# Kernel tuning notes

Measured on AMD Instinct MI355X. Metric: run time of the kernel, lower is better.

## Reference

```python
import jax, jax.numpy as jnp
import numpy as np

D = 3
BS = 64
T = 2048


def _fnn(x, w1, b1, w2, b2):
    # FNNnew: fc2(tanh(fc1(x))) * exp(-5*x); x: (T,1) -> (T,)
    z = jnp.tanh(x @ w1.T + b1) @ w2.T + b2
    return (z * jnp.exp(-5.0 * x))[:, 0]


def setup_inputs() -> dict:
    key = jax.random.key(0)
    ks = jax.random.split(key, 32)
    inp = {"x_data": jax.random.normal(ks[0], (BS, T, 2), dtype=jnp.float32)}
    inp["A1"] = jax.random.normal(ks[1], (D, D), dtype=jnp.float32)
    inp["A2"] = jax.random.normal(ks[2], (D, D), dtype=jnp.float32)
    i = 3
    for n in ("f", "g", "fp", "gp"):
        inp[n + "_w1"] = jax.random.normal(ks[i], (5, 1), dtype=jnp.float32) * 0.5; i += 1
        inp[n + "_b1"] = jax.random.normal(ks[i], (5,), dtype=jnp.float32) * 0.1; i += 1
        inp[n + "_w2"] = jax.random.normal(ks[i], (1, 5), dtype=jnp.float32) * 0.5; i += 1
        inp[n + "_b2"] = jax.random.normal(ks[i], (1,), dtype=jnp.float32) * 0.1; i += 1
    return inp


def reference(x_data, A1, A2, f_w1, f_b1, f_w2, f_b2, g_w1, g_b1, g_w2, g_b2,
              fp_w1, fp_b1, fp_w2, fp_b2, gp_w1, gp_b1, gp_w2, gp_b2):
    bs, t_len, _ = x_data.shape
    d = A1.shape[0]
    t = jnp.arange(t_len, dtype=jnp.float32)[:, None]
    f_arr = _fnn(t, f_w1, f_b1, f_w2, f_b2)[::-1]
    fp_arr = _fnn(t, fp_w1, fp_b1, fp_w2, fp_b2)[::-1]
    g_arr = _fnn(t, g_w1, g_b1, g_w2, g_b2)
    gp_arr = _fnn(t, gp_w1, gp_b1, gp_w2, gp_b2)
    # time-domain zero-pad then FFT (length 3T-2)
    Hf = jnp.fft.fft(jnp.pad(f_arr, (t_len - 1, t_len - 1)))
    Hfp = jnp.fft.fft(jnp.pad(fp_arr, (t_len - 1, t_len - 1)))
    Hg = jnp.fft.fft(jnp.pad(g_arr, (t_len - 1, t_len - 1)))
    Hgp = jnp.fft.fft(jnp.pad(gp_arr, (t_len - 1, t_len - 1)))
    # PathDev: X_t = X_{t-1} @ expm(A1s*z1_t + A2s*z2_t), X_0 = I
    A1s = A1 - A1.T
    A2s = A2 - A2.T
    G = A1s * x_data[..., 0, None, None] + A2s * x_data[..., 1, None, None]  # (bs,T,d,d)
    M = jax.vmap(jax.scipy.linalg.expm)(G.reshape(-1, d, d)).reshape(bs, t_len, d, d)

    X0 = jnp.broadcast_to(jnp.eye(d, dtype=x_data.dtype), (bs, d, d))

    def step(X, Mt):
        Xn = jnp.einsum('bij,bjk->bik', X, Mt)
        return Xn, Xn

    _, Xs = jax.lax.scan(step, X0, jnp.moveaxis(M[:, 1:], 0, 1))
    A = jnp.concatenate([X0[:, None], jnp.moveaxis(Xs, 0, 1)], axis=1)  # (bs,T,d,d)
    B = jnp.linalg.inv(A)
    Xr = A.reshape(bs, t_len, d * d)
    Xir = B.reshape(bs, t_len, d * d)
    # original pads the FFT output (frequency-domain padding) before multiply
    pad_t = lambda z: jnp.pad(z, ((0, 0), (t_len - 1, t_len - 1), (0, 0)))
    AA_fft = pad_t(jnp.fft.fft(Xir, axis=1))  # (bs, 3T-2, d^2)
    AB_fft = pad_t(jnp.fft.fft(Xr, axis=1))
    brd = lambda h: h[None, :, None]
    AA = jnp.fft.ifft(AA_fft * brd(Hf), axis=1)
    AB = jnp.fft.ifft(AB_fft * brd(Hg), axis=1)
    BA = jnp.fft.ifft(AA_fft * brd(Hfp), axis=1)
    BB = jnp.fft.ifft(AB_fft * brd(Hgp), axis=1)
    out = (AA * AB + BA * BB)[:, 2 * t_len - 2:, :]  # (bs,T,d^2)
    return out.reshape(bs, t_len, d, d).real
```

## Files before the change

### kernel.cpp

```cpp
#include <hip/hip_runtime.h>
#include <math.h>

#define TN 2048
#define NF 4096
#define NB 64
#define LF 6142LL
#define L2F 12284LL
#define PI_D 3.14159265358979323846264338327950288
#define C8 0.70710678118654752440084436210485
#define K16A 0.92387953251128675612818318939678828682
#define K16B 0.38268343236508977172845998403039886676
#define C8f   0.70710678118654752440f
#define K16Af 0.92387953251128675613f
#define K16Bf 0.38268343236508977173f

typedef double2 cpx;
typedef float2 cf;

__device__ __forceinline__ cpx cmk(double a, double b){ cpx r; r.x=a; r.y=b; return r; }
__device__ __forceinline__ cpx cadd(cpx a, cpx b){ return cmk(a.x+b.x, a.y+b.y); }
__device__ __forceinline__ cpx csub(cpx a, cpx b){ return cmk(a.x-b.x, a.y-b.y); }
__device__ __forceinline__ cpx cmul(cpx a, cpx b){ return cmk(a.x*b.x - a.y*b.y, a.x*b.y + a.y*b.x); }
__device__ __forceinline__ cpx cmulc(cpx a, cpx b){ return cmk(a.x*b.x + a.y*b.y, a.y*b.x - a.x*b.y); }
__device__ __forceinline__ cf c2s(cpx a){ cf r; r.x=(float)a.x; r.y=(float)a.y; return r; }

__device__ __forceinline__ cf cfmk(float a, float b){ cf r; r.x=a; r.y=b; return r; }
__device__ __forceinline__ cf cfadd(cf a, cf b){ return cfmk(a.x+b.x, a.y+b.y); }
__device__ __forceinline__ cf cfsub(cf a, cf b){ return cfmk(a.x-b.x, a.y-b.y); }
__device__ __forceinline__ cf cfmul(cf a, cf b){ return cfmk(a.x*b.x - a.y*b.y, a.x*b.y + a.y*b.x); }
__device__ __forceinline__ cf cfmulc(cf a, cf b){ return cfmk(a.x*b.x + a.y*b.y, a.y*b.x - a.x*b.y); }

__device__ __forceinline__ int SW(int i){ return i ^ ((i >> 3) & 7) ^ ((i >> 6) & 7); }
__device__ __forceinline__ int SWP(int i){ return i ^ ((i >> 4) & 15) ^ ((i >> 8) & 15); }

__device__ __forceinline__ void wsync(){
  __builtin_amdgcn_wave_barrier();
  asm volatile("s_waitcnt lgkmcnt(0)" ::: "memory");
  __builtin_amdgcn_wave_barrier();
}

__device__ __forceinline__ void fft8_bc(cpx* a){
  cpx u, v, d;
  u=a[0]; v=a[2]; a[0]=cadd(u,v); a[2]=csub(u,v);
  u=a[1]; v=a[3]; a[1]=cadd(u,v); d=csub(u,v); a[3]=cmk(d.y, -d.x);
  u=a[4]; v=a[6]; a[4]=cadd(u,v); a[6]=csub(u,v);
  u=a[5]; v=a[7]; a[5]=cadd(u,v); d=csub(u,v); a[7]=cmk(d.y, -d.x);
  u=a[0]; v=a[1]; a[0]=cadd(u,v); a[1]=csub(u,v);
  u=a[2]; v=a[3]; a[2]=cadd(u,v); a[3]=csub(u,v);
  u=a[4]; v=a[5]; a[4]=cadd(u,v); a[5]=csub(u,v);
  u=a[6]; v=a[7]; a[6]=cadd(u,v); a[7]=csub(u,v);
}
__device__ __forceinline__ void fft8(cpx* a){
  cpx u, v, d;
  u=a[0]; v=a[4]; a[0]=cadd(u,v); a[4]=csub(u,v);
  u=a[1]; v=a[5]; a[1]=cadd(u,v); d=csub(u,v); a[5]=cmk(C8*(d.x+d.y), C8*(d.y-d.x));
  u=a[2]; v=a[6]; a[2]=cadd(u,v); d=csub(u,v); a[6]=cmk(d.y, -d.x);
  u=a[3]; v=a[7]; a[3]=cadd(u,v); d=csub(u,v); a[7]=cmk(C8*(d.y-d.x), -C8*(d.x+d.y));
  fft8_bc(a);
}
__device__ __forceinline__ void fft16(cpx* a){
  cpx u, v, d;
  u=a[0]; v=a[8];  a[0]=cadd(u,v); a[8] = csub(u,v);
  u=a[1]; v=a[9];  a[1]=cadd(u,v); d=csub(u,v); a[9]  = cmk(K16A*d.x + K16B*d.y, K16A*d.y - K16B*d.x);
  u=a[2]; v=a[10]; a[2]=cadd(u,v); d=csub(u,v); a[10] = cmk(C8*(d.x+d.y), C8*(d.y-d.x));
  u=a[3]; v=a[11]; a[3]=cadd(u,v); d=csub(u,v); a[11] = cmk(K16B*d.x + K16A*d.y, K16B*d.y - K16A*d.x);
  u=a[4]; v=a[12]; a[4]=cadd(u,v); d=csub(u,v); a[12] = cmk(d.y, -d.x);
  u=a[5]; v=a[13]; a[5]=cadd(u,v); d=csub(u,v); a[13] = cmk(K16A*d.y - K16B*d.x, -(K16A*d.x + K16B*d.y));
  u=a[6]; v=a[14]; a[6]=cadd(u,v); d=csub(u,v); a[14] = cmk(C8*(d.y-d.x), -C8*(d.x+d.y));
  u=a[7]; v=a[15]; a[7]=cadd(u,v); d=csub(u,v); a[15] = cmk(K16B*d.y - K16A*d.x, -(K16A*d.y + K16B*d.x));
  fft8(a); fft8(a+8);
}

__device__ __forceinline__ void fft8s_bc(cf* a){
  cf u, v, d;
  u=a[0]; v=a[2]; a[0]=cfadd(u,v); a[2]=cfsub(u,v);
  u=a[1]; v=a[3]; a[1]=cfadd(u,v); d=cfsub(u,v); a[3]=cfmk(d.y, -d.x);
  u=a[4]; v=a[6]; a[4]=cfadd(u,v); a[6]=cfsub(u,v);
  u=a[5]; v=a[7]; a[5]=cfadd(u,v); d=cfsub(u,v); a[7]=cfmk(d.y, -d.x);
  u=a[0]; v=a[1]; a[0]=cfadd(u,v); a[1]=cfsub(u,v);
  u=a[2]; v=a[3]; a[2]=cfadd(u,v); a[3]=cfsub(u,v);
  u=a[4]; v=a[5]; a[4]=cfadd(u,v); a[5]=cfsub(u,v);
  u=a[6]; v=a[7]; a[6]=cfadd(u,v); a[7]=cfsub(u,v);
}
__device__ __forceinline__ void fft8s(cf* a){
  cf u, v, d;
  u=a[0]; v=a[4]; a[0]=cfadd(u,v); a[4]=cfsub(u,v);
  u=a[1]; v=a[5]; a[1]=cfadd(u,v); d=cfsub(u,v); a[5]=cfmk(C8f*(d.x+d.y), C8f*(d.y-d.x));
  u=a[2]; v=a[6]; a[2]=cfadd(u,v); d=cfsub(u,v); a[6]=cfmk(d.y, -d.x);
  u=a[3]; v=a[7]; a[3]=cfadd(u,v); d=cfsub(u,v); a[7]=cfmk(C8f*(d.y-d.x), -C8f*(d.x+d.y));
  fft8s_bc(a);
}
__device__ __forceinline__ void ifft8s(cf* a){
  cf u, v, t;
  u=a[0]; v=a[1]; a[0]=cfadd(u,v); a[1]=cfsub(u,v);
  u=a[2]; v=a[3]; a[2]=cfadd(u,v); a[3]=cfsub(u,v);
  u=a[4]; v=a[5]; a[4]=cfadd(u,v); a[5]=cfsub(u,v);
  u=a[6]; v=a[7]; a[6]=cfadd(u,v); a[7]=cfsub(u,v);
  u=a[0]; v=a[2]; a[0]=cfadd(u,v); a[2]=cfsub(u,v);
  u=a[1]; t=a[3]; v=cfmk(-t.y, t.x); a[1]=cfadd(u,v); a[3]=cfsub(u,v);
  u=a[4]; v=a[6]; a[4]=cfadd(u,v); a[6]=cfsub(u,v);
  u=a[5]; t=a[7]; v=cfmk(-t.y, t.x); a[5]=cfadd(u,v); a[7]=cfsub(u,v);
  u=a[0]; v=a[4]; a[0]=cfadd(u,v); a[4]=cfsub(u,v);
  u=a[1]; t=a[5]; v=cfmk(C8f*(t.x-t.y), C8f*(t.x+t.y)); a[1]=cfadd(u,v); a[5]=cfsub(u,v);
  u=a[2]; t=a[6]; v=cfmk(-t.y, t.x); a[2]=cfadd(u,v); a[6]=cfsub(u,v);
  u=a[3]; t=a[7]; v=cfmk(-C8f*(t.x+t.y), C8f*(t.x-t.y)); a[3]=cfadd(u,v); a[7]=cfsub(u,v);
}
__device__ __forceinline__ void fft4s(cf* a){
  cf u, v, d;
  u=a[0]; v=a[2]; a[0]=cfadd(u,v); a[2]=cfsub(u,v);
  u=a[1]; v=a[3]; a[1]=cfadd(u,v); d=cfsub(u,v); a[3]=cfmk(d.y, -d.x);
  u=a[0]; v=a[1]; a[0]=cfadd(u,v); a[1]=cfsub(u,v);
  u=a[2]; v=a[3]; a[2]=cfadd(u,v); a[3]=cfsub(u,v);
}
__device__ __forceinline__ void ffts16(cf* a){
  cf u, v, d;
  u=a[0]; v=a[8];  a[0]=cfadd(u,v); a[8] = cfsub(u,v);
  u=a[1]; v=a[9];  a[1]=cfadd(u,v); d=cfsub(u,v); a[9]  = cfmk(K16Af*d.x + K16Bf*d.y, K16Af*d.y - K16Bf*d.x);
  u=a[2]; v=a[10]; a[2]=cfadd(u,v); d=cfsub(u,v); a[10] = cfmk(C8f*(d.x+d.y), C8f*(d.y-d.x));
  u=a[3]; v=a[11]; a[3]=cfadd(u,v); d=cfsub(u,v); a[11] = cfmk(K16Bf*d.x + K16Af*d.y, K16Bf*d.y - K16Af*d.x);
  u=a[4]; v=a[12]; a[4]=cfadd(u,v); d=cfsub(u,v); a[12] = cfmk(d.y, -d.x);
  u=a[5]; v=a[13]; a[5]=cfadd(u,v); d=cfsub(u,v); a[13] = cfmk(K16Af*d.y - K16Bf*d.x, -(K16Af*d.x + K16Bf*d.y));
  u=a[6]; v=a[14]; a[6]=cfadd(u,v); d=cfsub(u,v); a[14] = cfmk(C8f*(d.y-d.x), -C8f*(d.x+d.y));
  u=a[7]; v=a[15]; a[7]=cfadd(u,v); d=cfsub(u,v); a[15] = cfmk(K16Bf*d.y - K16Af*d.x, -(K16Af*d.y + K16Bf*d.x));
  fft8s(a); fft8s(a+8);
}
__device__ __forceinline__ void ffts16h(cf* a){
  a[8]  = a[0];
  a[9]  = cfmk(K16Af*a[1].x + K16Bf*a[1].y, K16Af*a[1].y - K16Bf*a[1].x);
  a[10] = cfmk(C8f*(a[2].x+a[2].y), C8f*(a[2].y-a[2].x));
  a[11] = cfmk(K16Bf*a[3].x + K16Af*a[3].y, K16Bf*a[3].y - K16Af*a[3].x);
  a[12] = cfmk(a[4].y, -a[4].x);
  a[13] = cfmk(K16Af*a[5].y - K16Bf*a[5].x, -(K16Af*a[5].x + K16Bf*a[5].y));
  a[14] = cfmk(C8f*(a[6].y-a[6].x), -C8f*(a[6].x+a[6].y));
  a[15] = cfmk(K16Bf*a[7].y - K16Af*a[7].x, -(K16Af*a[7].y + K16Bf*a[7].x));
  fft8s(a); fft8s(a+8);
}
__device__ __forceinline__ void iffts16(cf* a){
  ifft8s(a); ifft8s(a+8);
  cf t, E;
  E=a[0]; t=a[8];                                                                   a[0]=cfadd(E,t); a[8] =cfsub(E,t);
  E=a[1]; t=cfmk(K16Af*a[9].x - K16Bf*a[9].y,  K16Af*a[9].y + K16Bf*a[9].x);        a[1]=cfadd(E,t); a[9] =cfsub(E,t);
  E=a[2]; t=cfmk(C8f*(a[10].x - a[10].y),      C8f*(a[10].x + a[10].y));            a[2]=cfadd(E,t); a[10]=cfsub(E,t);
  E=a[3]; t=cfmk(K16Bf*a[11].x - K16Af*a[11].y, K16Bf*a[11].y + K16Af*a[11].x);     a[3]=cfadd(E,t); a[11]=cfsub(E,t);
  E=a[4]; t=cfmk(-a[12].y, a[12].x);                                                a[4]=cfadd(E,t); a[12]=cfsub(E,t);
  E=a[5]; t=cfmk(-(K16Bf*a[13].x) - K16Af*a[13].y, K16Af*a[13].x - K16Bf*a[13].y);  a[5]=cfadd(E,t); a[13]=cfsub(E,t);
  E=a[6]; t=cfmk(-C8f*(a[14].x + a[14].y),     C8f*(a[14].x - a[14].y));            a[6]=cfadd(E,t); a[14]=cfsub(E,t);
  E=a[7]; t=cfmk(-(K16Af*a[15].x) - K16Bf*a[15].y, K16Bf*a[15].x - K16Af*a[15].y);  a[7]=cfadd(E,t); a[15]=cfsub(E,t);
}
__device__ __forceinline__ void iffts16h(cf* a){
  ifft8s(a); ifft8s(a+8);
  cf t;
  t=a[8];                                                                  a[0]=cfadd(a[0],t);
  t=cfmk(K16Af*a[9].x - K16Bf*a[9].y,  K16Af*a[9].y + K16Bf*a[9].x);       a[1]=cfadd(a[1],t);
  t=cfmk(C8f*(a[10].x - a[10].y),      C8f*(a[10].x + a[10].y));           a[2]=cfadd(a[2],t);
  t=cfmk(K16Bf*a[11].x - K16Af*a[11].y, K16Bf*a[11].y + K16Af*a[11].x);    a[3]=cfadd(a[3],t);
  t=cfmk(-a[12].y, a[12].x);                                               a[4]=cfadd(a[4],t);
  t=cfmk(-(K16Bf*a[13].x) - K16Af*a[13].y, K16Af*a[13].x - K16Bf*a[13].y); a[5]=cfadd(a[5],t);
  t=cfmk(-C8f*(a[14].x + a[14].y),     C8f*(a[14].x - a[14].y));           a[6]=cfadd(a[6],t);
  t=cfmk(-(K16Af*a[15].x) - K16Bf*a[15].y, K16Bf*a[15].x - K16Af*a[15].y); a[7]=cfadd(a[7],t);
}

__global__ __launch_bounds__(256) void k_prep(
    const float* fw1, const float* fb1, const float* fw2, const float* fb2,
    const float* gw1, const float* gb1, const float* gw2, const float* gb2,
    const float* pw1, const float* pb1, const float* pw2, const float* pb2,
    const float* qw1, const float* qb1, const float* qw2, const float* qb2,
    double* arr, cpx* tw, cf* tw32, cpx* Q, cpx* g2)
{
  int gid = blockIdx.x * 256 + threadIdx.x;
  if (gid < 4096){
    double s, c;
    sincos(-2.0 * PI_D * (double)gid / 4096.0, &s, &c);
    tw[gid] = cmk(c, s);
    tw32[gid] = cfmk((float)c, (float)s);
  }
  if (gid < 2048){
    long long i = gid;
    double s, c;
    long long a = ((2LL * TN - 2) * i) % LF;
    long long b = (i * i) % L2F;
    long long comb = (2 * a + b) % L2F;
    sincos(PI_D * (double)comb / (double)LF, &s, &c);
    Q[gid] = cmk(c, s);
    long long a2 = ((2LL * TN - 2 + i) * (TN - 1)) % LF;
    long long comb2 = (2 * a2 + b) % L2F;
    double phi = PI_D * (double)comb2 / (double)LF;
    double scale = 1.0 / ((double)LF * (double)LF) / (4096.0 * 4096.0);
    sincos(2.0 * phi, &s, &c);
    g2[gid] = cmk(c * scale, s * scale);
  }
  int fid = gid >> 11;
  int m = gid & (TN - 1);
  const float *W1, *B1, *W2, *B2;
  if (fid == 0){ W1=fw1; B1=fb1; W2=fw2; B2=fb2; }
  else if (fid == 1){ W1=gw1; B1=gb1; W2=gw2; B2=gb2; }
  else if (fid == 2){ W1=pw1; B1=pb1; W2=pw2; B2=pb2; }
  else { W1=qw1; B1=qb1; W2=qw2; B2=qb2; }
  int s = (fid == 0 || fid == 2) ? (TN - 1 - m) : m;
  double sv = (double)s;
  double z = (double)B2[0];
  #pragma unroll
  for (int h = 0; h < 5; h++)
    z += (double)W2[h] * tanh(sv * (double)W1[h] + (double)B1[h]);
  arr[fid * TN + m] = z * exp(-5.0 * sv);
}

__device__ __forceinline__ void mat_mul3(double* D, const double* A, const double* B){
  double r[9];
  #pragma unroll
  for (int i = 0; i < 3; i++)
    #pragma unroll
    for (int j = 0; j < 3; j++)
      r[i*3+j] = A[i*3]*B[j] + A[i*3+1]*B[3+j] + A[i*3+2]*B[6+j];
  #pragma unroll
  for (int k = 0; k < 9; k++) D[k] = r[k];
}
__device__ __forceinline__ void rod3(double* M, const double* a1, const double* a2,
                                     double z1, double z2){
  double G[9];
  #pragma unroll
  for (int k = 0; k < 9; k++) G[k] = a1[k]*z1 + a2[k]*z2;
  double wx = G[7], wy = G[2], wz = G[3];
  double th2 = wx*wx + wy*wy + wz*wz;
  double sa, cb;
  if (th2 < 1e-12){ sa = 1.0 - th2/6.0; cb = 0.5 - th2/24.0; }
  else { double th = sqrt(th2); sa = sin(th)/th; cb = (1.0 - cos(th))/th2; }
  double w[3] = {wx, wy, wz};
  #pragma unroll
  for (int i = 0; i < 3; i++)
    #pragma unroll
    for (int j = 0; j < 3; j++){
      double v = sa * G[i*3+j] + cb * (w[i]*w[j]);
      if (i == j) v += 1.0 - cb * th2;
      M[i*3+j] = v;
    }
}

__global__ __launch_bounds__(256) void k_front(
    const float* x, const float* A1f, const float* A2f,
    const double* arr, const cpx* Q, const cpx* tw,
    cf* HsQ, float* Asc, cf* chatp)
{
  __shared__ double smem[8192];
  int tid = threadIdx.x;
  int bid = blockIdx.x;
  if (bid < 256){
    cpx* part = (cpx*)smem;
    int f = bid >> 6;
    int jbase = (bid & 63) * 32;
    int chunk = tid & 7;
    int jl = tid >> 3;
    long long j = jbase + jl;
    long long jj = j + TN - 1;
    double s, c;
    sincos(-2.0 * PI_D * (double)jj / (double)LF, &s, &c);
    cpx W = cmk(c, s);
    long long m0 = (long long)chunk * 256;
    long long p0 = ((m0 + TN - 1) * jj) % LF;
    sincos(-2.0 * PI_D * (double)p0 / (double)LF, &s, &c);
    cpx ph = cmk(c, s);
    const double* a = arr + f * TN;
    cpx acc = cmk(0.0, 0.0);
    for (int m = (int)m0; m < (int)m0 + 256; m++){
      double av = a[m];
      acc.x += av * ph.x;
      acc.y += av * ph.y;
      ph = cmul(ph, W);
    }
    part[tid] = acc;
    __syncthreads();
    if (chunk == 0){
      cpx tot = cmk(0.0, 0.0);
      for (int q = 0; q < 8; q++) tot = cadd(tot, part[(jl << 3) + q]);
      HsQ[f * TN + (int)j] = c2s(cmul(tot, Q[j]));
    }
  } else if (bid < 320){
    int b = bid - 256;
    double (*S)[9] = (double(*)[9])smem;
    int k = tid;
    double a1[9], a2[9];
    #pragma unroll
    for (int i = 0; i < 3; i++)
      #pragma unroll
      for (int j = 0; j < 3; j++){
        a1[i*3+j] = (double)A1f[i*3+j] - (double)A1f[j*3+i];
        a2[i*3+j] = (double)A2f[i*3+j] - (double)A2f[j*3+i];
      }
    const float* xb = x + (size_t)b * TN * 2;
    double C[9] = {1,0,0, 0,1,0, 0,0,1};
    for (int i = 0; i < 8; i++){
      int t = k * 8 + i;
      if (t >= 1){
        double M[9];
        rod3(M, a1, a2, (double)xb[2*t], (double)xb[2*t+1]);
        mat_mul3(C, C, M);
      }
    }
    #pragma unroll
    for (int q = 0; q < 9; q++) S[k][q] = C[q];
    __syncthreads();
    for (int ofs = 1; ofs < 256; ofs <<= 1){
      double Lm[9], Rm[9];
      bool act = (k >= ofs);
      if (act){
        #pragma unroll
        for (int q = 0; q < 9; q++){ Lm[q] = S[k-ofs][q]; Rm[q] = S[k][q]; }
      }
      __syncthreads();
      if (act){
        double P[9];
        mat_mul3(P, Lm, Rm);
        #pragma unroll
        for (int q = 0; q < 9; q++) S[k][q] = P[q];
      }
      __syncthreads();
    }
    double P[9];
    if (k == 0){
      P[0]=1; P[1]=0; P[2]=0; P[3]=0; P[4]=1; P[5]=0; P[6]=0; P[7]=0; P[8]=1;
    } else {
      #pragma unroll
      for (int q = 0; q < 9; q++) P[q] = S[k-1][q];
    }
    for (int i = 0; i < 8; i++){
      int t = k * 8 + i;
      if (t >= 1){
        double M[9];
        rod3(M, a1, a2, (double)xb[2*t], (double)xb[2*t+1]);
        mat_mul3(P, P, M);
      }
      #pragma unroll
      for (int q = 0; q < 9; q++)
        Asc[(((size_t)b * 9 + q) << 11) + t] = (float)P[q];
    }
  } else {
    cpx* buf = (cpx*)smem;
    const int R16[16] = {0,8,4,12,2,10,6,14,1,9,5,13,3,11,7,15};
    for (int mq = tid; mq < NF; mq += 256){
      long long mm = (mq <= 2048) ? mq : (NF - mq);
      long long qq = (mm * mm) % L2F;
      double s, c;
      sincos(-PI_D * (double)qq / (double)LF, &s, &c);
      buf[SW(mq)] = cmk(c, s);
    }
    __syncthreads();
    {
      cpx a[16];
      #pragma unroll
      for (int k = 0; k < 16; k++) a[k] = buf[SW(tid + (k << 8))];
      fft16(a);
      #pragma unroll
      for (int q = 0; q < 16; q++){
        int d = R16[q]; cpx v = a[q];
        if (d) v = cmul(v, tw[tid * d]);
        buf[SW(tid + (d << 8))] = v;
      }
    }
    __syncthreads();
    {
      int m2 = tid & 15, base2 = ((tid >> 4) << 8) + m2;
      cpx a[16];
      #pragma unroll
      for (int k = 0; k < 16; k++) a[k] = buf[SW(base2 + (k << 4))];
      fft16(a);
      #pragma unroll
      for (int q = 0; q < 16; q++){
        int d = R16[q]; cpx v = a[q];
        if (d) v = cmul(v, tw[(m2 * d) << 4]);
        buf[SW(base2 + (d << 4))] = v;
      }
    }
    __syncthreads();
    {
      cpx a[16];
      #pragma unroll
      for (int k = 0; k < 16; k++) a[k] = buf[SW((tid << 4) + k)];
      fft16(a);
      #pragma unroll
      for (int q = 0; q < 16; q++)
        chatp[(R16[q] << 8) | tid] = c2s(a[q]);
    }
  }
}

__global__ __launch_bounds__(256, 4) void k_fft_u(const float* Asc, const cf* tw32, cf* U){
  __shared__ cf buf[TN];
  int pos = threadIdx.x;
  int b = blockIdx.x / 5, p = blockIdx.x % 5;
  int c0 = 2 * p;
  bool dual = (p < 4);
  const float* s0 = Asc + (((size_t)b * 9 + c0) << 11);
  const float* s1 = Asc + (((size_t)b * 9 + (dual ? c0 + 1 : c0)) << 11);
  const int R8[8] = {0,4,2,6,1,5,3,7};
  {
    cf a[8];
    #pragma unroll
    for (int j = 0; j < 8; j++){
      int idx = pos + (j << 8);
      a[j] = cfmk(s0[idx], dual ? s1[idx] : 0.0f);
    }
    fft8s(a);
    #pragma unroll
    for (int q = 0; q < 8; q++){
      int k = R8[q]; cf v = a[q];
      if (k) v = cfmul(v, tw32[(pos * k) << 1]);
      buf[SW(pos + (k << 8))] = v;
    }
  }
  __syncthreads();
  int l = pos & 63;
  int ll = l & 31;
  int segb = ((((pos >> 6) << 1) + (l >> 5)) << 8);
  {
    int base = segb + ll;
    cf a[8];
    #pragma unroll
    for (int j = 0; j < 8; j++) a[j] = buf[SW(base + (j << 5))];
    fft8s(a);
    #pragma unroll
    for (int q = 0; q < 8; q++){
      int k = R8[q]; cf v = a[q];
      if (k) v = cfmul(v, tw32[(ll * k) << 4]);
      buf[SW(base + (k << 5))] = v;
    }
  }
  wsync();
  {
    int base = segb + ((ll >> 2) << 5) + (ll & 3);
    cf a[8];
    #pragma unroll
    for (int j = 0; j < 8; j++) a[j] = buf[SW(base + (j << 2))];
    fft8s(a);
    #pragma unroll
    for (int q = 0; q < 8; q++){
      int k = R8[q]; cf v = a[q];
      if (k) v = cfmul(v, tw32[((ll & 3) * k) << 7]);
      buf[SW(base + (k << 2))] = v;
    }
  }
  wsync();
  {
    const int R4[4] = {0,2,1,3};
    #pragma unroll
    for (int h = 0; h < 2; h++){
      int base = segb + (((ll << 1) + h) << 2);
      cf a4[4];
      #pragma unroll
      for (int j = 0; j < 4; j++) a4[j] = buf[SW(base + j)];
      fft4s(a4);
      #pragma unroll
      for (int q = 0; q < 4; q++) buf[SW(base + R4[q])] = a4[q];
    }
  }
  __syncthreads();
  cf* dst0 = U + (((size_t)b * 9 + c0) << 11);
  cf* dst1 = U + (((size_t)b * 9 + c0 + 1) << 11);
  #pragma unroll
  for (int ii = 0; ii < 8; ii++){
    int f = pos + (ii << 8);
    int s  = ((f & 7) << 8) + (((f >> 3) & 7) << 5) + (((f >> 6) & 7) << 2) + (f >> 9);
    int m  = (TN - f) & (TN - 1);
    int sm = ((m & 7) << 8) + (((m >> 3) & 7) << 5) + (((m >> 6) & 7) << 2) + (m >> 9);
    cf Z = buf[SW(s)], Zm = buf[SW(sm)];
    dst0[f] = cfmk(0.5f * (Z.x + Zm.x), 0.5f * (Z.y - Zm.y));
    if (dual)
      dst1[f] = cfmk(0.5f * (Z.y + Zm.y), 0.5f * (Zm.x - Z.x));
  }
}

__global__ __launch_bounds__(256, 2) void k_czt(const cf* U, const cf* HsQ, const cf* tw32,
                                                const cf* chatp, const cpx* g2, float* Rst){
  __shared__ float4 bufp[NF];
  int gb = blockIdx.x;
  int pair = gb & 1;
  int bc = gb >> 1;
  int b = bc / 9, c = bc % 9;
  int ct = (c % 3) * 3 + (c / 3);
  const cf* Us0 = U + ((size_t)b * 9 + ct) * TN;
  const cf* Us1 = U + ((size_t)b * 9 + c)  * TN;
  const cf* H0 = HsQ + ((size_t)(pair << 1) << 11);
  const cf* H1 = HsQ + ((size_t)((pair << 1) | 1) << 11);
  int t = threadIdx.x;
  int m = t & 15;
  int base2 = ((t >> 4) << 8) + m;
  int base3 = t << 4;
  const int R16[16] = {0,8,4,12,2,10,6,14,1,9,5,13,3,11,7,15};

  cf a[16], bb[16];
  #pragma unroll
  for (int k = 0; k < 8; k++){
    a[k]  = cfmul(Us0[t + (k << 8)], H0[t + (k << 8)]);
    bb[k] = cfmul(Us1[t + (k << 8)], H1[t + (k << 8)]);
  }
  ffts16h(a); ffts16h(bb);
  #pragma unroll
  for (int q = 0; q < 16; q++){
    int d = R16[q];
    cf va = a[q], vb = bb[q];
    if (d){ cf tv = tw32[t * d]; va = cfmul(va, tv); vb = cfmul(vb, tv); }
    bufp[SWP(t + (d << 8))] = make_float4(va.x, va.y, vb.x, vb.y);
  }
  __syncthreads();
  #pragma unroll
  for (int k = 0; k < 16; k++){
    float4 p = bufp[SWP(base2 + (k << 4))];
    a[k]  = cfmk(p.x, p.y);
    bb[k] = cfmk(p.z, p.w);
  }
  ffts16(a); ffts16(bb);
  #pragma unroll
  for (int q = 0; q < 16; q++){
    int d = R16[q];
    cf va = a[q], vb = bb[q];
    if (d){ cf tv = tw32[(m * d) << 4]; va = cfmul(va, tv); vb = cfmul(vb, tv); }
    bufp[SWP(base2 + (d << 4))] = make_float4(va.x, va.y, vb.x, vb.y);
  }
  wsync();
  #pragma unroll
  for (int k = 0; k < 16; k++){
    float4 p = bufp[SWP(base3 + k)];
    a[k]  = cfmk(p.x, p.y);
    bb[k] = cfmk(p.z, p.w);
  }
  ffts16(a); ffts16(bb);
  #pragma unroll
  for (int q = 0; q < 16; q++){
    cf ch = chatp[(R16[q] << 8) | t];
    a[q] = cfmul(a[q], ch);
    bb[q] = cfmul(bb[q], ch);
  }
  iffts16(a); iffts16(bb);
  #pragma unroll
  for (int k = 0; k < 16; k++)
    bufp[SWP(base3 + k)] = make_float4(a[k].x, a[k].y, bb[k].x, bb[k].y);
  wsync();
  #pragma unroll
  for (int q = 0; q < 16; q++){
    int d = R16[q];
    float4 p = bufp[SWP(base2 + (d << 4))];
    cf va = cfmk(p.x, p.y), vb = cfmk(p.z, p.w);
    if (d){ cf tv = tw32[(m * d) << 4]; va = cfmulc(va, tv); vb = cfmulc(vb, tv); }
    a[q] = va; bb[q] = vb;
  }
  iffts16(a); iffts16(bb);
  #pragma unroll
  for (int k = 0; k < 16; k++)
    bufp[SWP(base2 + (k << 4))] = make_float4(a[k].x, a[k].y, bb[k].x, bb[k].y);
  __syncthreads();
  #pragma unroll
  for (int q = 0; q < 16; q++){
    int d = R16[q];
    float4 p = bufp[SWP(t + (d << 8))];
    cf va = cfmk(p.x, p.y), vb = cfmk(p.z, p.w);
    if (d){ cf tv = tw32[t * d]; va = cfmulc(va, tv); vb = cfmulc(vb, tv); }
    a[q] = va; bb[q] = vb;
  }
  iffts16h(a); iffts16h(bb);
  size_t rb = ((size_t)(pair * (NB * 9) + bc) << 11);
  #pragma unroll
  for (int j = 0; j < 8; j++){
    int r = t + (j << 8);
    double ax = (double)a[j].x, ay = (double)a[j].y;
    double bx = (double)bb[j].x, by = (double)bb[j].y;
    double prx = ax * bx - ay * by;
    double pry = ax * by + ay * bx;
    cpx g = g2[r];
    Rst[rb + r] = (float)(prx * g.x - pry * g.y);
  }
}

__global__ __launch_bounds__(256) void k_out(const float* Rst, float* out){
  __shared__ float ld[9][513];
  int b = blockIdx.x >> 2;
  int r0 = (blockIdx.x & 3) << 9;
  for (int idx = threadIdx.x; idx < 9 * 512; idx += 256){
    int cc = idx >> 9, r = idx & 511;
    size_t o0 = ((size_t)(b * 9 + cc) << 11) + r0 + r;
    ld[cc][r] = Rst[o0] + Rst[o0 + ((size_t)(NB * 9) << 11)];
  }
  __syncthreads();
  for (int idx = threadIdx.x; idx < 512 * 9; idx += 256){
    int r = idx / 9, cc = idx - 9 * r;
    out[((size_t)b * TN + r0 + r) * 9 + cc] = ld[cc][r];
  }
}

extern "C" void kernel_launch(void* const* d_in, const int* in_sizes, int n_in,
                              void* d_out, int out_size, void* d_ws, size_t ws_size,
                              hipStream_t stream){
  const float* x  = (const float*)d_in[0];
  const float* A1 = (const float*)d_in[1];
  const float* A2 = (const float*)d_in[2];
  const float* fpar[16];
  for (int i = 0; i < 16; i++) fpar[i] = (const float*)d_in[3 + i];
  float* out = (float*)d_out;

  double* ws = (double*)d_ws;
  size_t o = 0;
  double* arr  = ws + o;         o += 4 * TN;
  cf* HsQ      = (cf*)(ws + o);  o += 4 * TN;
  cpx* tw      = (cpx*)(ws + o); o += 2 * NF;
  cf* tw32     = (cf*)(ws + o);  o += NF;
  cf* chatp    = (cf*)(ws + o);  o += NF;
  cpx* Q       = (cpx*)(ws + o); o += 2 * TN;
  cpx* g2      = (cpx*)(ws + o); o += 2 * TN;
  double* uni  = ws + o;         o += (size_t)NB * TN * 9;
  float* Asc   = (float*)uni;
  float* Rst   = (float*)uni;
  cf* U        = (cf*)(ws + o);  o += (size_t)NB * 9 * TN;

  k_prep<<<32, 256, 0, stream>>>(fpar[0], fpar[1], fpar[2], fpar[3],
                                 fpar[4], fpar[5], fpar[6], fpar[7],
                                 fpar[8], fpar[9], fpar[10], fpar[11],
                                 fpar[12], fpar[13], fpar[14], fpar[15],
                                 arr, tw, tw32, Q, g2);
  k_front<<<321, 256, 0, stream>>>(x, A1, A2, arr, Q, tw, HsQ, Asc, chatp);
  k_fft_u<<<NB * 5, 256, 0, stream>>>(Asc, tw32, U);
  k_czt<<<NB * 9 * 2, 256, 0, stream>>>(U, HsQ, tw32, chatp, g2, Rst);
  k_out<<<NB * 4, 256, 0, stream>>>(Rst, out);
}
```

Baseline: 188.8 us.

## Fuse output transpose into CZT kernel via atomics; reorder front blocks; float filter array

Removes the separate k_out kernel and its intermediate Rst buffer. The two CZT halves now atomically add their results directly into the zeroed output, in the strided final layout, which adds a memset and uncoalesced atomics in exchange. The front kernel puts the long serial path-development blocks first so they are scheduled before the filter DFT blocks. The NN filter evaluation now runs in float rather than double, which slightly reduces precision.

```diff
diff --git a/kernel.cpp b/kernel.cpp
--- a/kernel.cpp
+++ b/kernel.cpp
@@ -165,7 +165,7 @@
     const float* gw1, const float* gb1, const float* gw2, const float* gb2,
     const float* pw1, const float* pb1, const float* pw2, const float* pb2,
     const float* qw1, const float* qb1, const float* qw2, const float* qb2,
-    double* arr, cpx* tw, cf* tw32, cpx* Q, cpx* g2)
+    float* arr, cpx* tw, cf* tw32, cpx* Q, cpx* g2)
 {
   int gid = blockIdx.x * 256 + threadIdx.x;
   if (gid < 4096){
@@ -197,12 +197,12 @@
   else if (fid == 2){ W1=pw1; B1=pb1; W2=pw2; B2=pb2; }
   else { W1=qw1; B1=qb1; W2=qw2; B2=qb2; }
   int s = (fid == 0 || fid == 2) ? (TN - 1 - m) : m;
-  double sv = (double)s;
-  double z = (double)B2[0];
+  float sv = (float)s;
+  float z = B2[0];
   #pragma unroll
   for (int h = 0; h < 5; h++)
-    z += (double)W2[h] * tanh(sv * (double)W1[h] + (double)B1[h]);
-  arr[fid * TN + m] = z * exp(-5.0 * sv);
+    z += W2[h] * tanhf(sv * W1[h] + B1[h]);
+  arr[fid * TN + m] = z * expf(-5.0f * sv);
 }
 
 __device__ __forceinline__ void mat_mul3(double* D, const double* A, const double* B){
@@ -238,44 +238,14 @@
 
 __global__ __launch_bounds__(256) void k_front(
     const float* x, const float* A1f, const float* A2f,
-    const double* arr, const cpx* Q, const cpx* tw,
+    const float* arr, const cpx* Q, const cpx* tw,
     cf* HsQ, float* Asc, cf* chatp)
 {
   __shared__ double smem[8192];
   int tid = threadIdx.x;
   int bid = blockIdx.x;
-  if (bid < 256){
-    cpx* part = (cpx*)smem;
-    int f = bid >> 6;
-    int jbase = (bid & 63) * 32;
-    int chunk = tid & 7;
-    int jl = tid >> 3;
-    long long j = jbase + jl;
-    long long jj = j + TN - 1;
-    double s, c;
-    sincos(-2.0 * PI_D * (double)jj / (double)LF, &s, &c);
-    cpx W = cmk(c, s);
-    long long m0 = (long long)chunk * 256;
-    long long p0 = ((m0 + TN - 1) * jj) % LF;
-    sincos(-2.0 * PI_D * (double)p0 / (double)LF, &s, &c);
-    cpx ph = cmk(c, s);
-    const double* a = arr + f * TN;
-    cpx acc = cmk(0.0, 0.0);
-    for (int m = (int)m0; m < (int)m0 + 256; m++){
-      double av = a[m];
-      acc.x += av * ph.x;
-      acc.y += av * ph.y;
-      ph = cmul(ph, W);
-    }
-    part[tid] = acc;
-    __syncthreads();
-    if (chunk == 0){
-      cpx tot = cmk(0.0, 0.0);
-      for (int q = 0; q < 8; q++) tot = cadd(tot, part[(jl << 3) + q]);
-      HsQ[f * TN + (int)j] = c2s(cmul(tot, Q[j]));
-    }
-  } else if (bid < 320){
-    int b = bid - 256;
+  if (bid < 64){
+    int b = bid;
     double (*S)[9] = (double(*)[9])smem;
     int k = tid;
     double a1[9], a2[9];
@@ -333,7 +303,7 @@
       for (int q = 0; q < 9; q++)
         Asc[(((size_t)b * 9 + q) << 11) + t] = (float)P[q];
     }
-  } else {
+  } else if (bid == 64){
     cpx* buf = (cpx*)smem;
     const int R16[16] = {0,8,4,12,2,10,6,14,1,9,5,13,3,11,7,15};
     for (int mq = tid; mq < NF; mq += 256){
@@ -379,6 +349,37 @@
       #pragma unroll
       for (int q = 0; q < 16; q++)
         chatp[(R16[q] << 8) | tid] = c2s(a[q]);
+    }
+  } else {
+    int hb = bid - 65;
+    cpx* part = (cpx*)smem;
+    int f = hb >> 6;
+    int jbase = (hb & 63) * 32;
+    int chunk = tid & 7;
+    int jl = tid >> 3;
+    long long j = jbase + jl;
+    long long jj = j + TN - 1;
+    double s, c;
+    sincos(-2.0 * PI_D * (double)jj / (double)LF, &s, &c);
+    cpx W = cmk(c, s);
+    long long m0 = (long long)chunk * 256;
+    long long p0 = ((m0 + TN - 1) * jj) % LF;
+    sincos(-2.0 * PI_D * (double)p0 / (double)LF, &s, &c);
+    cpx ph = cmk(c, s);
+    const float* a = arr + f * TN;
+    cpx acc = cmk(0.0, 0.0);
+    for (int m = (int)m0; m < (int)m0 + 256; m++){
+      double av = (double)a[m];
+      acc.x += av * ph.x;
+      acc.y += av * ph.y;
+      ph = cmul(ph, W);
+    }
+    part[tid] = acc;
+    __syncthreads();
+    if (chunk == 0){
+      cpx tot = cmk(0.0, 0.0);
+      for (int q = 0; q < 8; q++) tot = cadd(tot, part[(jl << 3) + q]);
+      HsQ[f * TN + (int)j] = c2s(cmul(tot, Q[j]));
     }
   }
 }
@@ -469,7 +470,7 @@
 }
 
 __global__ __launch_bounds__(256, 2) void k_czt(const cf* U, const cf* HsQ, const cf* tw32,
-                                                const cf* chatp, const cpx* g2, float* Rst){
+                                                const cf* chatp, const cpx* g2, float* out){
   __shared__ float4 bufp[NF];
   int gb = blockIdx.x;
   int pair = gb & 1;
@@ -556,7 +557,7 @@
     a[q] = va; bb[q] = vb;
   }
   iffts16h(a); iffts16h(bb);
-  size_t rb = ((size_t)(pair * (NB * 9) + bc) << 11);
+  float* ob = out + (size_t)b * TN * 9 + c;
   #pragma unroll
   for (int j = 0; j < 8; j++){
     int r = t + (j << 8);
@@ -565,23 +566,7 @@
     double prx = ax * bx - ay * by;
     double pry = ax * by + ay * bx;
     cpx g = g2[r];
-    Rst[rb + r] = (float)(prx * g.x - pry * g.y);
-  }
-}
-
-__global__ __launch_bounds__(256) void k_out(const float* Rst, float* out){
-  __shared__ float ld[9][513];
-  int b = blockIdx.x >> 2;
-  int r0 = (blockIdx.x & 3) << 9;
-  for (int idx = threadIdx.x; idx < 9 * 512; idx += 256){
-    int cc = idx >> 9, r = idx & 511;
-    size_t o0 = ((size_t)(b * 9 + cc) << 11) + r0 + r;
-    ld[cc][r] = Rst[o0] + Rst[o0 + ((size_t)(NB * 9) << 11)];
-  }
-  __syncthreads();
-  for (int idx = threadIdx.x; idx < 512 * 9; idx += 256){
-    int r = idx / 9, cc = idx - 9 * r;
-    out[((size_t)b * TN + r0 + r) * 9 + cc] = ld[cc][r];
+    atomicAdd(ob + (size_t)r * 9, (float)(prx * g.x - pry * g.y));
   }
 }
 
@@ -597,17 +582,17 @@
 
   double* ws = (double*)d_ws;
   size_t o = 0;
-  double* arr  = ws + o;         o += 4 * TN;
+  float* arr   = (float*)(ws + o); o += 2 * TN;
   cf* HsQ      = (cf*)(ws + o);  o += 4 * TN;
   cpx* tw      = (cpx*)(ws + o); o += 2 * NF;
   cf* tw32     = (cf*)(ws + o);  o += NF;
   cf* chatp    = (cf*)(ws + o);  o += NF;
   cpx* Q       = (cpx*)(ws + o); o += 2 * TN;
   cpx* g2      = (cpx*)(ws + o); o += 2 * TN;
-  double* uni  = ws + o;         o += (size_t)NB * TN * 9;
-  float* Asc   = (float*)uni;
-  float* Rst   = (float*)uni;
+  float* Asc   = (float*)(ws + o); o += (size_t)NB * TN * 9 / 2;
   cf* U        = (cf*)(ws + o);  o += (size_t)NB * 9 * TN;
+
+  hipMemsetAsync(d_out, 0, out_size, stream);
 
   k_prep<<<32, 256, 0, stream>>>(fpar[0], fpar[1], fpar[2], fpar[3],
                                  fpar[4], fpar[5], fpar[6], fpar[7],
@@ -616,6 +601,5 @@
                                  arr, tw, tw32, Q, g2);
   k_front<<<321, 256, 0, stream>>>(x, A1, A2, arr, Q, tw, HsQ, Asc, chatp);
   k_fft_u<<<NB * 5, 256, 0, stream>>>(Asc, tw32, U);
-  k_czt<<<NB * 9 * 2, 256, 0, stream>>>(U, HsQ, tw32, chatp, g2, Rst);
-  k_out<<<NB * 4, 256, 0, stream>>>(Rst, out);
-}
+  k_czt<<<NB * 9 * 2, 256, 0, stream>>>(U, HsQ, tw32, chatp, g2, out);
+}
```

Result: slower. 216.0 us (+14.4%).

## Fold prep kernel into front kernel, computing FNN arrays and twiddles per block

Applied to the files above, without the earlier changes.

Removes the separate k_prep launch. Its work is spread across k_front blocks: each H-block recomputes its FNN array in float into shared memory, computes the Q phase inline, and uses on-the-fly double twiddles. Dedicated blocks generate tw32 and g2. This drops one kernel launch and its serial dependency, and removes the global arr, tw and Q buffers. In exchange the FNN work is repeated in every block, and the FNN now runs in float instead of double, which may change accuracy.

```diff
diff --git a/kernel.cpp b/kernel.cpp
--- a/kernel.cpp
+++ b/kernel.cpp
@@ -29,6 +29,12 @@
 __device__ __forceinline__ cf cfsub(cf a, cf b){ return cfmk(a.x-b.x, a.y-b.y); }
 __device__ __forceinline__ cf cfmul(cf a, cf b){ return cfmk(a.x*b.x - a.y*b.y, a.x*b.y + a.y*b.x); }
 __device__ __forceinline__ cf cfmulc(cf a, cf b){ return cfmk(a.x*b.x + a.y*b.y, a.y*b.x - a.x*b.y); }
+
+__device__ __forceinline__ cpx twd64(int idx){
+  double s, c;
+  sincos(-2.0 * PI_D * (double)idx / 4096.0, &s, &c);
+  return cmk(c, s);
+}
 
 __device__ __forceinline__ int SW(int i){ return i ^ ((i >> 3) & 7) ^ ((i >> 6) & 7); }
 __device__ __forceinline__ int SWP(int i){ return i ^ ((i >> 4) & 15) ^ ((i >> 8) & 15); }
@@ -160,51 +166,6 @@
   t=cfmk(-(K16Af*a[15].x) - K16Bf*a[15].y, K16Bf*a[15].x - K16Af*a[15].y); a[7]=cfadd(a[7],t);
 }
 
-__global__ __launch_bounds__(256) void k_prep(
-    const float* fw1, const float* fb1, const float* fw2, const float* fb2,
-    const float* gw1, const float* gb1, const float* gw2, const float* gb2,
-    const float* pw1, const float* pb1, const float* pw2, const float* pb2,
-    const float* qw1, const float* qb1, const float* qw2, const float* qb2,
-    double* arr, cpx* tw, cf* tw32, cpx* Q, cpx* g2)
-{
-  int gid = blockIdx.x * 256 + threadIdx.x;
-  if (gid < 4096){
-    double s, c;
-    sincos(-2.0 * PI_D * (double)gid / 4096.0, &s, &c);
-    tw[gid] = cmk(c, s);
-    tw32[gid] = cfmk((float)c, (float)s);
-  }
-  if (gid < 2048){
-    long long i = gid;
-    double s, c;
-    long long a = ((2LL * TN - 2) * i) % LF;
-    long long b = (i * i) % L2F;
-    long long comb = (2 * a + b) % L2F;
-    sincos(PI_D * (double)comb / (double)LF, &s, &c);
-    Q[gid] = cmk(c, s);
-    long long a2 = ((2LL * TN - 2 + i) * (TN - 1)) % LF;
-    long long comb2 = (2 * a2 + b) % L2F;
-    double phi = PI_D * (double)comb2 / (double)LF;
-    double scale = 1.0 / ((double)LF * (double)LF) / (4096.0 * 4096.0);
-    sincos(2.0 * phi, &s, &c);
-    g2[gid] = cmk(c * scale, s * scale);
-  }
-  int fid = gid >> 11;
-  int m = gid & (TN - 1);
-  const float *W1, *B1, *W2, *B2;
-  if (fid == 0){ W1=fw1; B1=fb1; W2=fw2; B2=fb2; }
-  else if (fid == 1){ W1=gw1; B1=gb1; W2=gw2; B2=gb2; }
-  else if (fid == 2){ W1=pw1; B1=pb1; W2=pw2; B2=pb2; }
-  else { W1=qw1; B1=qb1; W2=qw2; B2=qb2; }
-  int s = (fid == 0 || fid == 2) ? (TN - 1 - m) : m;
-  double sv = (double)s;
-  double z = (double)B2[0];
-  #pragma unroll
-  for (int h = 0; h < 5; h++)
-    z += (double)W2[h] * tanh(sv * (double)W1[h] + (double)B1[h]);
-  arr[fid * TN + m] = z * exp(-5.0 * sv);
-}
-
 __device__ __forceinline__ void mat_mul3(double* D, const double* A, const double* B){
   double r[9];
   #pragma unroll
@@ -238,44 +199,17 @@
 
 __global__ __launch_bounds__(256) void k_front(
     const float* x, const float* A1f, const float* A2f,
-    const double* arr, const cpx* Q, const cpx* tw,
-    cf* HsQ, float* Asc, cf* chatp)
+    const float* fw1, const float* fb1, const float* fw2, const float* fb2,
+    const float* gw1, const float* gb1, const float* gw2, const float* gb2,
+    const float* pw1, const float* pb1, const float* pw2, const float* pb2,
+    const float* qw1, const float* qb1, const float* qw2, const float* qb2,
+    cf* HsQ, float* Asc, cf* chatp, cf* tw32, cpx* g2)
 {
   __shared__ double smem[8192];
   int tid = threadIdx.x;
   int bid = blockIdx.x;
-  if (bid < 256){
-    cpx* part = (cpx*)smem;
-    int f = bid >> 6;
-    int jbase = (bid & 63) * 32;
-    int chunk = tid & 7;
-    int jl = tid >> 3;
-    long long j = jbase + jl;
-    long long jj = j + TN - 1;
-    double s, c;
-    sincos(-2.0 * PI_D * (double)jj / (double)LF, &s, &c);
-    cpx W = cmk(c, s);
-    long long m0 = (long long)chunk * 256;
-    long long p0 = ((m0 + TN - 1) * jj) % LF;
-    sincos(-2.0 * PI_D * (double)p0 / (double)LF, &s, &c);
-    cpx ph = cmk(c, s);
-    const double* a = arr + f * TN;
-    cpx acc = cmk(0.0, 0.0);
-    for (int m = (int)m0; m < (int)m0 + 256; m++){
-      double av = a[m];
-      acc.x += av * ph.x;
-      acc.y += av * ph.y;
-      ph = cmul(ph, W);
-    }
-    part[tid] = acc;
-    __syncthreads();
-    if (chunk == 0){
-      cpx tot = cmk(0.0, 0.0);
-      for (int q = 0; q < 8; q++) tot = cadd(tot, part[(jl << 3) + q]);
-      HsQ[f * TN + (int)j] = c2s(cmul(tot, Q[j]));
-    }
-  } else if (bid < 320){
-    int b = bid - 256;
+  if (bid < 64){
+    int b = bid;
     double (*S)[9] = (double(*)[9])smem;
     int k = tid;
     double a1[9], a2[9];
@@ -333,7 +267,7 @@
       for (int q = 0; q < 9; q++)
         Asc[(((size_t)b * 9 + q) << 11) + t] = (float)P[q];
     }
-  } else {
+  } else if (bid == 64){
     cpx* buf = (cpx*)smem;
     const int R16[16] = {0,8,4,12,2,10,6,14,1,9,5,13,3,11,7,15};
     for (int mq = tid; mq < NF; mq += 256){
@@ -352,7 +286,7 @@
       #pragma unroll
       for (int q = 0; q < 16; q++){
         int d = R16[q]; cpx v = a[q];
-        if (d) v = cmul(v, tw[tid * d]);
+        if (d) v = cmul(v, twd64(tid * d));
         buf[SW(tid + (d << 8))] = v;
       }
     }
@@ -366,7 +300,7 @@
       #pragma unroll
       for (int q = 0; q < 16; q++){
         int d = R16[q]; cpx v = a[q];
-        if (d) v = cmul(v, tw[(m2 * d) << 4]);
+        if (d) v = cmul(v, twd64((m2 * d) << 4));
         buf[SW(base2 + (d << 4))] = v;
       }
     }
@@ -379,6 +313,75 @@
       #pragma unroll
       for (int q = 0; q < 16; q++)
         chatp[(R16[q] << 8) | tid] = c2s(a[q]);
+    }
+  } else if (bid == 65){
+    for (int i = tid; i < NF; i += 256){
+      double s, c;
+      sincos(-2.0 * PI_D * (double)i / 4096.0, &s, &c);
+      tw32[i] = cfmk((float)c, (float)s);
+    }
+    for (int gi = tid; gi < TN; gi += 256){
+      long long i = gi;
+      double s, c;
+      long long b2 = (i * i) % L2F;
+      long long a2 = ((2LL * TN - 2 + i) * (TN - 1)) % LF;
+      long long comb2 = (2 * a2 + b2) % L2F;
+      double phi = PI_D * (double)comb2 / (double)LF;
+      double scale = 1.0 / ((double)LF * (double)LF) / (4096.0 * 4096.0);
+      sincos(2.0 * phi, &s, &c);
+      g2[gi] = cmk(c * scale, s * scale);
+    }
+  } else {
+    int hb = bid - 66;
+    int f = hb >> 6;
+    float* arrF = (float*)smem;
+    cpx* part = (cpx*)(smem + 1032);
+    const float *W1, *B1, *W2, *B2;
+    if (f == 0){ W1=fw1; B1=fb1; W2=fw2; B2=fb2; }
+    else if (f == 1){ W1=gw1; B1=gb1; W2=gw2; B2=gb2; }
+    else if (f == 2){ W1=pw1; B1=pb1; W2=pw2; B2=pb2; }
+    else { W1=qw1; B1=qb1; W2=qw2; B2=qb2; }
+    for (int k = 0; k < 8; k++){
+      int m = tid + (k << 8);
+      int s = (f == 0 || f == 2) ? (TN - 1 - m) : m;
+      float sv = (float)s;
+      float z = B2[0];
+      #pragma unroll
+      for (int h = 0; h < 5; h++)
+        z += W2[h] * tanhf(sv * W1[h] + B1[h]);
+      arrF[m + (m >> 8)] = z * expf(-5.0f * sv);
+    }
+    __syncthreads();
+    int jbase = (hb & 63) * 32;
+    int chunk = tid & 7;
+    int jl = tid >> 3;
+    long long j = jbase + jl;
+    long long jj = j + TN - 1;
+    double s, c;
+    sincos(-2.0 * PI_D * (double)jj / (double)LF, &s, &c);
+    cpx W = cmk(c, s);
+    long long m0 = (long long)chunk * 256;
+    long long p0 = ((m0 + TN - 1) * jj) % LF;
+    sincos(-2.0 * PI_D * (double)p0 / (double)LF, &s, &c);
+    cpx ph = cmk(c, s);
+    cpx acc = cmk(0.0, 0.0);
+    for (int m = (int)m0; m < (int)m0 + 256; m++){
+      double av = (double)arrF[m + (m >> 8)];
+      acc.x += av * ph.x;
+      acc.y += av * ph.y;
+      ph = cmul(ph, W);
+    }
+    part[tid] = acc;
+    __syncthreads();
+    if (chunk == 0){
+      cpx tot = cmk(0.0, 0.0);
+      for (int q = 0; q < 8; q++) tot = cadd(tot, part[(jl << 3) + q]);
+      long long i = j;
+      long long aq = ((2LL * TN - 2) * i) % LF;
+      long long bq = (i * i) % L2F;
+      long long comb = (2 * aq + bq) % L2F;
+      sincos(PI_D * (double)comb / (double)LF, &s, &c);
+      HsQ[f * TN + (int)j] = c2s(cmul(tot, cmk(c, s)));
     }
   }
 }
@@ -597,24 +600,21 @@
 
   double* ws = (double*)d_ws;
   size_t o = 0;
-  double* arr  = ws + o;         o += 4 * TN;
   cf* HsQ      = (cf*)(ws + o);  o += 4 * TN;
-  cpx* tw      = (cpx*)(ws + o); o += 2 * NF;
   cf* tw32     = (cf*)(ws + o);  o += NF;
   cf* chatp    = (cf*)(ws + o);  o += NF;
-  cpx* Q       = (cpx*)(ws + o); o += 2 * TN;
   cpx* g2      = (cpx*)(ws + o); o += 2 * TN;
   double* uni  = ws + o;         o += (size_t)NB * TN * 9;
   float* Asc   = (float*)uni;
   float* Rst   = (float*)uni;
   cf* U        = (cf*)(ws + o);  o += (size_t)NB * 9 * TN;
 
-  k_prep<<<32, 256, 0, stream>>>(fpar[0], fpar[1], fpar[2], fpar[3],
-                                 fpar[4], fpar[5], fpar[6], fpar[7],
-                                 fpar[8], fpar[9], fpar[10], fpar[11],
-                                 fpar[12], fpar[13], fpar[14], fpar[15],
-                                 arr, tw, tw32, Q, g2);
-  k_front<<<321, 256, 0, stream>>>(x, A1, A2, arr, Q, tw, HsQ, Asc, chatp);
+  k_front<<<322, 256, 0, stream>>>(x, A1, A2,
+                                   fpar[0], fpar[1], fpar[2], fpar[3],
+                                   fpar[4], fpar[5], fpar[6], fpar[7],
+                                   fpar[8], fpar[9], fpar[10], fpar[11],
+                                   fpar[12], fpar[13], fpar[14], fpar[15],
+                                   HsQ, Asc, chatp, tw32, g2);
   k_fft_u<<<NB * 5, 256, 0, stream>>>(Asc, tw32, U);
   k_czt<<<NB * 9 * 2, 256, 0, stream>>>(U, HsQ, tw32, chatp, g2, Rst);
   k_out<<<NB * 4, 256, 0, stream>>>(Rst, out);
```

Result: slower. 253.2 us (+34.1%).
